# Optimization experiments

Measured on AMD Instinct MI355X. Metric: run time of the kernel, lower is better.

## Reference

```python
import jax, jax.numpy as jnp
import numpy as np

B, C, H, W = 8, 64, 128, 128


def setup_inputs() -> dict:
    key = jax.random.key(0)
    k1, k2, k3 = jax.random.split(key, 3)
    x = jax.random.normal(k1, (B, C, H, W), dtype=jnp.float32)
    # offset conv weights: (2C, C, 3, 3), small init like the module (std=0.01)
    W_off = jax.random.normal(k2, (2 * C, C, 3, 3), dtype=jnp.float32) * 0.01
    # following regular conv: (C_out, C, 3, 3)
    W_conv = jax.random.normal(k3, (C, C, 3, 3), dtype=jnp.float32) * 0.05
    b_conv = jnp.zeros((C,), dtype=jnp.float32)
    return {"x": x, "W_off": W_off, "W_conv": W_conv, "b_conv": b_conv}


def _conv2d_same(x, w):
    return jax.lax.conv_general_dilated(
        x, w, window_strides=(1, 1), padding=[(1, 1), (1, 1)],
        dimension_numbers=("NCHW", "OIHW", "NCHW"))


def _deform_offset(x, W_off):
    """Faithful ConvOffset2D: offset conv + clamped 4-corner bilinear gather."""
    b, c, h, w = x.shape
    offsets_ = _conv2d_same(x, W_off)                    # (b, 2c, h, w)
    # torch contiguous view (b,2c,h,w) -> (b*c, h*w, 2): adjacent w elements
    # become the 2 offset components; jnp.reshape matches this exactly.
    offsets = offsets_.reshape(b * c, h * w, 2)
    xf = x.reshape(b * c, h, w)

    gy, gx = jnp.meshgrid(jnp.arange(h), jnp.arange(w), indexing="ij")
    grid = jnp.stack([gy, gx], axis=-1).reshape(-1, 2).astype(x.dtype)  # (h*w, 2)
    coords = offsets + grid[None]                        # (b*c, h*w, 2)

    cy = jnp.clip(coords[..., 0], 0.0, h - 1)
    cx = jnp.clip(coords[..., 1], 0.0, w - 1)
    y0 = jnp.floor(cy)
    y1 = jnp.ceil(cy)
    x0 = jnp.floor(cx)
    x1 = jnp.ceil(cx)

    flat = xf.reshape(-1)                                # (b*c*h*w,)
    base = (jnp.arange(b * c, dtype=jnp.int32) * (h * w))[:, None]

    def gather(yy, xx):
        idx = base + yy.astype(jnp.int32) * w + xx.astype(jnp.int32)
        return flat[idx]

    v_lt = gather(y0, x0)   # (floor y, floor x)
    v_rb = gather(y1, x1)   # (ceil y,  ceil x)
    v_lb = gather(y0, x1)   # (floor y, ceil x)
    v_rt = gather(y1, x0)   # (ceil y,  floor x)

    dy = cy - y0
    dx = cx - x0
    v_t = dy * (v_rt - v_lt) + v_lt
    v_b = dy * (v_rb - v_lb) + v_lb
    out = dx * (v_b - v_t) + v_t                         # (b*c, h*w)
    return out.reshape(b, c, h, w)


def reference(x, W_off, W_conv, b_conv):
    x_def = _deform_offset(x, W_off)
    out = _conv2d_same(x_def, W_conv) + b_conv[None, :, None, None]
    return out
```

## Files before the change

### kernel.cpp

```cpp
#include <hip/hip_runtime.h>

#define DH 128
#define DW 128
#define DB 8
#define DC 64
constexpr int HW = DH * DW;

typedef __attribute__((ext_vector_type(4))) float f32x4;
typedef __attribute__((ext_vector_type(16))) float f32x16;
typedef __attribute__((ext_vector_type(8))) short bf16x8;
typedef __attribute__((ext_vector_type(4))) unsigned int u32x4;

__device__ __forceinline__ unsigned short f2b(float f) {
    unsigned int u = __builtin_bit_cast(unsigned int, f);
    u = (u + 0x7FFFu + ((u >> 16) & 1u)) >> 16;
    return (unsigned short)u;
}
__device__ __forceinline__ float b2f(unsigned short h) {
    unsigned int u = ((unsigned int)h) << 16;
    return __builtin_bit_cast(float, u);
}

__global__ __launch_bounds__(256) void xpose_kernel(
    const float* __restrict__ x, unsigned short* __restrict__ xh)
{
    __shared__ unsigned short sm[64 * 80];
    const int b = blockIdx.y;
    const int p0 = blockIdx.x * 64;
    const int t = threadIdx.x;
    const int ci = t >> 2, q = t & 3;
    const float* xr = x + ((size_t)b * 64 + ci) * HW + p0;
#pragma unroll
    for (int j = 0; j < 4; ++j) {
        int pix = (j * 4 + q) * 4;
        float4 v = *(const float4*)(xr + pix);
        sm[(pix + 0) * 80 + ci] = f2b(v.x);
        sm[(pix + 1) * 80 + ci] = f2b(v.y);
        sm[(pix + 2) * 80 + ci] = f2b(v.z);
        sm[(pix + 3) * 80 + ci] = f2b(v.w);
    }
    __syncthreads();
    unsigned short* outp = xh + ((size_t)b * HW + p0) * 64;
    for (int i = t; i < 512; i += 256) {
        int pix = i >> 3, cq = i & 7;
        u32x4 v = *(const u32x4*)(sm + pix * 80 + cq * 8);
        *(u32x4*)(outp + pix * 64 + cq * 8) = v;
    }
}

__global__ __launch_bounds__(256) void wprep_kernel(
    const float* __restrict__ wo, const float* __restrict__ wc,
    unsigned short* __restrict__ wt1, unsigned short* __restrict__ wt2)
{
    int id = blockIdx.x * 256 + threadIdx.x;
    const int N1 = 9 * 128 * 64, N2 = 9 * 64 * 64;
    if (id < N1) {
        int t = id / (128 * 64);
        int rem = id - t * 128 * 64;
        int co = rem >> 6, ci = rem & 63;
        wt1[id] = f2b(wo[(co * 64 + ci) * 9 + t]);
    } else if (id < N1 + N2) {
        int k = id - N1;
        int t = k / (64 * 64);
        int rem = k - t * 64 * 64;
        int co = rem >> 6, ci = rem & 63;
        wt2[k] = f2b(wc[(co * 64 + ci) * 9 + t]);
    }
}

template<int COUT, int MI, bool HWC_BF16_OUT>
__global__ __launch_bounds__(512, 4) void conv_mfma_kernel(
    const unsigned short* __restrict__ xh,
    const unsigned short* __restrict__ wt,
    const float* __restrict__ bias,
    void* __restrict__ outp)
{
    constexpr int WBYTES = COUT * 64 * 2;
    constexpr int SPASS = WBYTES / 8192;
    __shared__ char sm[41472 + 2 * WBYTES];
    char* const wbuf0 = sm + 41472;
    char* const wbuf1 = sm + 41472 + WBYTES;

    const int tid = threadIdx.x;
    const int b = blockIdx.y;
    const int ty0 = (blockIdx.x >> 3) << 4;
    const int tx0 = (blockIdx.x & 7) << 4;
    const unsigned short* xb = xh + (size_t)b * HW * 64;

    u32x4 wreg[SPASS];
    {
        const char* wsrc = (const char*)wt;
#pragma unroll
        for (int s = 0; s < SPASS; ++s) {
            int L = (s * 512 + tid) * 16;
            wreg[s] = *(const u32x4*)(wsrc + (L ^ (((L >> 7) & 7) << 4)));
        }
    }
    for (int i = tid; i < 2592; i += 512) {
        int hp = i >> 3, cq = i & 7;
        int hy = hp / 18, hx = hp - hy * 18;
        int gy = ty0 + hy - 1, gx = tx0 + hx - 1;
        u32x4 v = {0u, 0u, 0u, 0u};
        if ((unsigned)gy < 128u && (unsigned)gx < 128u)
            v = *(const u32x4*)(xb + (size_t)((gy << 7) + gx) * 64 + cq * 8);
        *(u32x4*)(sm + ((hp * 128 + cq * 16) ^ ((hp & 7) << 4))) = v;
    }
#pragma unroll
    for (int s = 0; s < SPASS; ++s) {
        int L = (s * 512 + tid) * 16;
        *(u32x4*)(wbuf0 + L) = wreg[s];
    }
    __syncthreads();

    const int lane = tid & 63;
    const int wv = tid >> 6;
    const int wm = wv & 1;
    const int wn = wv >> 1;
    const int n = lane & 31;
    const int half = lane >> 5;
    const int px = n & 15;
    const int pyb = wn * 4 + (n >> 4);
    const int swzA = (lane & 7) << 4;
    const int rowA = (wm * (MI * 32) + n) * 128 + half * 16;

    int hp0[2];
#pragma unroll
    for (int ni = 0; ni < 2; ++ni)
        hp0[ni] = (pyb + ni * 2) * 18 + px;

    f32x16 acc[MI][2];
#pragma unroll
    for (int mi = 0; mi < MI; ++mi)
#pragma unroll
        for (int ni = 0; ni < 2; ++ni)
#pragma unroll
            for (int e = 0; e < 16; ++e) acc[mi][ni][e] = 0.f;

#pragma unroll
    for (int t9 = 0; t9 < 9; ++t9) {
        const int toff = (t9 / 3) * 18 + (t9 % 3);
        const char* wb = (t9 & 1) ? wbuf1 : wbuf0;
        u32x4 wr[SPASS];
        if (t9 < 8) {
            const char* wsrc = (const char*)(wt + (size_t)(t9 + 1) * COUT * 64);
#pragma unroll
            for (int s = 0; s < SPASS; ++s) {
                int L = (s * 512 + tid) * 16;
                wr[s] = *(const u32x4*)(wsrc + (L ^ (((L >> 7) & 7) << 4)));
            }
        }
#pragma unroll
        for (int kk = 0; kk < 4; ++kk) {
            const int kcol = kk * 32;
            bf16x8 a[MI], bv[2];
#pragma unroll
            for (int mi = 0; mi < MI; ++mi)
                a[mi] = *(const bf16x8*)(wb + ((rowA + mi * 4096 + kcol) ^ swzA));
#pragma unroll
            for (int ni = 0; ni < 2; ++ni) {
                int hp = hp0[ni] + toff;
                bv[ni] = *(const bf16x8*)(sm + ((hp * 128 + kcol + half * 16) ^ ((hp & 7) << 4)));
            }
#pragma unroll
            for (int mi = 0; mi < MI; ++mi)
#pragma unroll
                for (int ni = 0; ni < 2; ++ni)
                    acc[mi][ni] = __builtin_amdgcn_mfma_f32_32x32x16_bf16(
                        a[mi], bv[ni], acc[mi][ni], 0, 0, 0);
        }
        if (t9 < 8) {
            char* wbn = ((t9 + 1) & 1) ? wbuf1 : wbuf0;
#pragma unroll
            for (int s = 0; s < SPASS; ++s) {
                int L = (s * 512 + tid) * 16;
                *(u32x4*)(wbn + L) = wr[s];
            }
        }
        __syncthreads();
    }

#pragma unroll
    for (int ni = 0; ni < 2; ++ni) {
        int py = pyb + ni * 2;
        int gp = (ty0 + py) * 128 + tx0 + px;
        if (HWC_BF16_OUT) {
            unsigned short* o = (unsigned short*)outp + ((size_t)b * HW + gp) * COUT;
#pragma unroll
            for (int mi = 0; mi < MI; ++mi) {
                int cob = wm * (MI * 32) + mi * 32 + half * 4;
#pragma unroll
                for (int g = 0; g < 4; ++g) {
                    uint2 pk;
                    pk.x = (unsigned)f2b(acc[mi][ni][g * 4 + 0]) |
                           ((unsigned)f2b(acc[mi][ni][g * 4 + 1]) << 16);
                    pk.y = (unsigned)f2b(acc[mi][ni][g * 4 + 2]) |
                           ((unsigned)f2b(acc[mi][ni][g * 4 + 3]) << 16);
                    *(uint2*)(o + cob + g * 8) = pk;
                }
            }
        } else {
            float* o = (float*)outp + (size_t)b * COUT * HW + gp;
#pragma unroll
            for (int mi = 0; mi < MI; ++mi) {
                int cob = wm * (MI * 32) + mi * 32 + half * 4;
#pragma unroll
                for (int g = 0; g < 4; ++g)
#pragma unroll
                    for (int r = 0; r < 4; ++r) {
                        int co = cob + g * 8 + r;
                        o[(size_t)co * HW] = acc[mi][ni][g * 4 + r] + bias[co];
                    }
            }
        }
    }
}

__global__ __launch_bounds__(256) void deform_kernel(
    const unsigned short* __restrict__ xh,
    const unsigned short* __restrict__ offs,
    unsigned short* __restrict__ xdef)
{
    int idx = blockIdx.x * 256 + threadIdx.x;
    int ci = idx & 63;
    int bp = idx >> 6;
    int p = bp & (HW - 1);
    int b = bp >> 14;
    int ch = 2 * ci + (p >> 13);
    int pp = (2 * p) & (HW - 1);
    const unsigned short* ob = offs + (size_t)b * HW * 128;
    float oy = b2f(ob[(size_t)pp * 128 + ch]);
    float ox = b2f(ob[(size_t)(pp + 1) * 128 + ch]);
    int gy = p >> 7, gx = p & 127;
    float cy = fminf(fmaxf(oy + (float)gy, 0.f), 127.f);
    float cx = fminf(fmaxf(ox + (float)gx, 0.f), 127.f);
    float y0f = floorf(cy), x0f = floorf(cx);
    int y0 = (int)y0f, x0i = (int)x0f;
    int y1 = (int)ceilf(cy), x1 = (int)ceilf(cx);
    const unsigned short* pl = xh + (size_t)b * HW * 64 + ci;
    float v_lt = b2f(pl[(size_t)(y0 * 128 + x0i) * 64]);
    float v_rb = b2f(pl[(size_t)(y1 * 128 + x1) * 64]);
    float v_lb = b2f(pl[(size_t)(y0 * 128 + x1) * 64]);
    float v_rt = b2f(pl[(size_t)(y1 * 128 + x0i) * 64]);
    float dy = cy - y0f, dx = cx - x0f;
    float v_t = fmaf(dy, v_rt - v_lt, v_lt);
    float v_b = fmaf(dy, v_rb - v_lb, v_lb);
    xdef[(size_t)bp * 64 + ci] = f2b(fmaf(dx, v_b - v_t, v_t));
}

extern "C" void kernel_launch(void* const* d_in, const int* in_sizes, int n_in,
                              void* d_out, int out_size, void* d_ws, size_t ws_size,
                              hipStream_t stream) {
    const float* x      = (const float*)d_in[0];
    const float* W_off  = (const float*)d_in[1];
    const float* W_conv = (const float*)d_in[2];
    const float* b_conv = (const float*)d_in[3];

    unsigned short* xh   = (unsigned short*)d_ws;
    unsigned short* offs = xh + (size_t)DB * HW * 64;
    unsigned short* xdef = offs + (size_t)DB * HW * 128;
    unsigned short* wt1  = xdef + (size_t)DB * HW * 64;
    unsigned short* wt2  = wt1 + 9 * 128 * 64;
    float* out = (float*)d_out;

    xpose_kernel<<<dim3(HW / 64, DB), 256, 0, stream>>>(x, xh);
    wprep_kernel<<<(9 * 128 * 64 + 9 * 64 * 64 + 255) / 256, 256, 0, stream>>>(
        W_off, W_conv, wt1, wt2);

    conv_mfma_kernel<128, 2, true><<<dim3(64, DB), 512, 0, stream>>>(
        xh, wt1, nullptr, offs);

    deform_kernel<<<(DB * HW * 64) / 256, 256, 0, stream>>>(xh, offs, xdef);

    conv_mfma_kernel<64, 1, false><<<dim3(64, DB), 512, 0, stream>>>(
        xdef, wt2, b_conv, out);
}
```

Measured before the change: 162.2 us.

## Fuse deformable bilinear sampling into second conv and merge prep kernels

The bilinear deformable gather now runs inside the second MFMA conv kernel, which writes the sampled halo tile straight into shared memory instead of going through a global xdef buffer. The transpose and weight-prep kernels are merged into one launch. This removes a global write and read of the deformed tensor plus two kernel launches. The cost is that halo pixels are recomputed per tile (18x18 for a 16x16 output), and the conv kernel's staging now does gather-heavy scattered loads.

```diff
diff --git a/kernel.cpp b/kernel.cpp
--- a/kernel.cpp
+++ b/kernel.cpp
@@ -21,50 +21,50 @@
     return __builtin_bit_cast(float, u);
 }
 
-__global__ __launch_bounds__(256) void xpose_kernel(
-    const float* __restrict__ x, unsigned short* __restrict__ xh)
-{
-    __shared__ unsigned short sm[64 * 80];
-    const int b = blockIdx.y;
-    const int p0 = blockIdx.x * 64;
-    const int t = threadIdx.x;
-    const int ci = t >> 2, q = t & 3;
-    const float* xr = x + ((size_t)b * 64 + ci) * HW + p0;
-#pragma unroll
-    for (int j = 0; j < 4; ++j) {
-        int pix = (j * 4 + q) * 4;
-        float4 v = *(const float4*)(xr + pix);
-        sm[(pix + 0) * 80 + ci] = f2b(v.x);
-        sm[(pix + 1) * 80 + ci] = f2b(v.y);
-        sm[(pix + 2) * 80 + ci] = f2b(v.z);
-        sm[(pix + 3) * 80 + ci] = f2b(v.w);
-    }
-    __syncthreads();
-    unsigned short* outp = xh + ((size_t)b * HW + p0) * 64;
-    for (int i = t; i < 512; i += 256) {
-        int pix = i >> 3, cq = i & 7;
-        u32x4 v = *(const u32x4*)(sm + pix * 80 + cq * 8);
-        *(u32x4*)(outp + pix * 64 + cq * 8) = v;
-    }
-}
-
-__global__ __launch_bounds__(256) void wprep_kernel(
-    const float* __restrict__ wo, const float* __restrict__ wc,
+__global__ __launch_bounds__(256) void prep_kernel(
+    const float* __restrict__ x, const float* __restrict__ wo,
+    const float* __restrict__ wc, unsigned short* __restrict__ xh,
     unsigned short* __restrict__ wt1, unsigned short* __restrict__ wt2)
 {
-    int id = blockIdx.x * 256 + threadIdx.x;
-    const int N1 = 9 * 128 * 64, N2 = 9 * 64 * 64;
-    if (id < N1) {
-        int t = id / (128 * 64);
-        int rem = id - t * 128 * 64;
-        int co = rem >> 6, ci = rem & 63;
-        wt1[id] = f2b(wo[(co * 64 + ci) * 9 + t]);
-    } else if (id < N1 + N2) {
-        int k = id - N1;
-        int t = k / (64 * 64);
-        int rem = k - t * 64 * 64;
-        int co = rem >> 6, ci = rem & 63;
-        wt2[k] = f2b(wc[(co * 64 + ci) * 9 + t]);
+    __shared__ unsigned short smx[64 * 80];
+    const int blk = blockIdx.x;
+    const int t = threadIdx.x;
+    if (blk < 2048) {
+        const int b = blk >> 8;
+        const int p0 = (blk & 255) * 64;
+        const int ci = t >> 2, q = t & 3;
+        const float* xr = x + ((size_t)b * 64 + ci) * HW + p0;
+#pragma unroll
+        for (int j = 0; j < 4; ++j) {
+            int pix = (j * 4 + q) * 4;
+            float4 v = *(const float4*)(xr + pix);
+            smx[(pix + 0) * 80 + ci] = f2b(v.x);
+            smx[(pix + 1) * 80 + ci] = f2b(v.y);
+            smx[(pix + 2) * 80 + ci] = f2b(v.z);
+            smx[(pix + 3) * 80 + ci] = f2b(v.w);
+        }
+        __syncthreads();
+        unsigned short* outp = xh + ((size_t)b * HW + p0) * 64;
+        for (int i = t; i < 512; i += 256) {
+            int pix = i >> 3, cq = i & 7;
+            u32x4 v = *(const u32x4*)(smx + pix * 80 + cq * 8);
+            *(u32x4*)(outp + pix * 64 + cq * 8) = v;
+        }
+    } else {
+        int id = (blk - 2048) * 256 + t;
+        const int N1 = 9 * 128 * 64, N2 = 9 * 64 * 64;
+        if (id < N1) {
+            int tp = id / (128 * 64);
+            int rem = id - tp * 128 * 64;
+            int co = rem >> 6, ci = rem & 63;
+            wt1[id] = f2b(wo[(co * 64 + ci) * 9 + tp]);
+        } else if (id < N1 + N2) {
+            int k = id - N1;
+            int tp = k / (64 * 64);
+            int rem = k - tp * 64 * 64;
+            int co = rem >> 6, ci = rem & 63;
+            wt2[k] = f2b(wc[(co * 64 + ci) * 9 + tp]);
+        }
     }
 }
 
@@ -215,36 +215,129 @@
     }
 }
 
-__global__ __launch_bounds__(256) void deform_kernel(
+__global__ __launch_bounds__(512, 4) void conv2_deform_kernel(
     const unsigned short* __restrict__ xh,
     const unsigned short* __restrict__ offs,
-    unsigned short* __restrict__ xdef)
+    const unsigned short* __restrict__ wt,
+    const float* __restrict__ bias,
+    float* __restrict__ out)
 {
-    int idx = blockIdx.x * 256 + threadIdx.x;
-    int ci = idx & 63;
-    int bp = idx >> 6;
-    int p = bp & (HW - 1);
-    int b = bp >> 14;
-    int ch = 2 * ci + (p >> 13);
-    int pp = (2 * p) & (HW - 1);
+    __shared__ char sm[41472 + 2 * 8192];
+    char* const wbuf0 = sm + 41472;
+    char* const wbuf1 = sm + 41472 + 8192;
+
+    const int tid = threadIdx.x;
+    const int b = blockIdx.y;
+    const int ty0 = (blockIdx.x >> 3) << 4;
+    const int tx0 = (blockIdx.x & 7) << 4;
+    const unsigned short* xb = xh + (size_t)b * HW * 64;
     const unsigned short* ob = offs + (size_t)b * HW * 128;
-    float oy = b2f(ob[(size_t)pp * 128 + ch]);
-    float ox = b2f(ob[(size_t)(pp + 1) * 128 + ch]);
-    int gy = p >> 7, gx = p & 127;
-    float cy = fminf(fmaxf(oy + (float)gy, 0.f), 127.f);
-    float cx = fminf(fmaxf(ox + (float)gx, 0.f), 127.f);
-    float y0f = floorf(cy), x0f = floorf(cx);
-    int y0 = (int)y0f, x0i = (int)x0f;
-    int y1 = (int)ceilf(cy), x1 = (int)ceilf(cx);
-    const unsigned short* pl = xh + (size_t)b * HW * 64 + ci;
-    float v_lt = b2f(pl[(size_t)(y0 * 128 + x0i) * 64]);
-    float v_rb = b2f(pl[(size_t)(y1 * 128 + x1) * 64]);
-    float v_lb = b2f(pl[(size_t)(y0 * 128 + x1) * 64]);
-    float v_rt = b2f(pl[(size_t)(y1 * 128 + x0i) * 64]);
-    float dy = cy - y0f, dx = cx - x0f;
-    float v_t = fmaf(dy, v_rt - v_lt, v_lt);
-    float v_b = fmaf(dy, v_rb - v_lb, v_lb);
-    xdef[(size_t)bp * 64 + ci] = f2b(fmaf(dx, v_b - v_t, v_t));
+
+    u32x4 wreg;
+    {
+        int L = tid * 16;
+        wreg = *(const u32x4*)((const char*)wt + (L ^ (((L >> 7) & 7) << 4)));
+    }
+
+    for (int i = tid; i < 324 * 64; i += 512) {
+        int hp = i >> 6, ci = i & 63;
+        int hy = hp / 18, hx = hp - hy * 18;
+        int gy = ty0 + hy - 1, gx = tx0 + hx - 1;
+        unsigned short val = 0;
+        if ((unsigned)gy < 128u && (unsigned)gx < 128u) {
+            int q = (gy << 7) + gx;
+            int ch = 2 * ci + (q >> 13);
+            int pp = (2 * q) & (HW - 1);
+            float oy = b2f(ob[(size_t)pp * 128 + ch]);
+            float ox = b2f(ob[(size_t)(pp + 1) * 128 + ch]);
+            float cy = fminf(fmaxf(oy + (float)gy, 0.f), 127.f);
+            float cx = fminf(fmaxf(ox + (float)gx, 0.f), 127.f);
+            float y0f = floorf(cy), x0f = floorf(cx);
+            int y0 = (int)y0f, x0i = (int)x0f;
+            int y1 = (int)ceilf(cy), x1 = (int)ceilf(cx);
+            const unsigned short* pl = xb + ci;
+            float v_lt = b2f(pl[(size_t)(y0 * 128 + x0i) * 64]);
+            float v_rb = b2f(pl[(size_t)(y1 * 128 + x1) * 64]);
+            float v_lb = b2f(pl[(size_t)(y0 * 128 + x1) * 64]);
+            float v_rt = b2f(pl[(size_t)(y1 * 128 + x0i) * 64]);
+            float dy = cy - y0f, dxf = cx - x0f;
+            float v_t = fmaf(dy, v_rt - v_lt, v_lt);
+            float v_b = fmaf(dy, v_rb - v_lb, v_lb);
+            val = f2b(fmaf(dxf, v_b - v_t, v_t));
+        }
+        *(unsigned short*)(sm + ((hp * 128 + ci * 2) ^ ((hp & 7) << 4))) = val;
+    }
+    *(u32x4*)(wbuf0 + tid * 16) = wreg;
+    __syncthreads();
+
+    const int lane = tid & 63;
+    const int wv = tid >> 6;
+    const int wm = wv & 1;
+    const int wn = wv >> 1;
+    const int n = lane & 31;
+    const int half = lane >> 5;
+    const int px = n & 15;
+    const int pyb = wn * 4 + (n >> 4);
+    const int swzA = (lane & 7) << 4;
+    const int rowA = (wm * 32 + n) * 128 + half * 16;
+
+    int hp0[2];
+#pragma unroll
+    for (int ni = 0; ni < 2; ++ni)
+        hp0[ni] = (pyb + ni * 2) * 18 + px;
+
+    f32x16 acc[2];
+#pragma unroll
+    for (int ni = 0; ni < 2; ++ni)
+#pragma unroll
+        for (int e = 0; e < 16; ++e) acc[ni][e] = 0.f;
+
+#pragma unroll
+    for (int t9 = 0; t9 < 9; ++t9) {
+        const int toff = (t9 / 3) * 18 + (t9 % 3);
+        const char* wb = (t9 & 1) ? wbuf1 : wbuf0;
+        u32x4 wr;
+        if (t9 < 8) {
+            const char* wsrc = (const char*)(wt + (size_t)(t9 + 1) * 64 * 64);
+            int L = tid * 16;
+            wr = *(const u32x4*)(wsrc + (L ^ (((L >> 7) & 7) << 4)));
+        }
+#pragma unroll
+        for (int kk = 0; kk < 4; ++kk) {
+            const int kcol = kk * 32;
+            bf16x8 a = *(const bf16x8*)(wb + ((rowA + kcol) ^ swzA));
+            bf16x8 bv[2];
+#pragma unroll
+            for (int ni = 0; ni < 2; ++ni) {
+                int hp = hp0[ni] + toff;
+                bv[ni] = *(const bf16x8*)(sm + ((hp * 128 + kcol + half * 16) ^ ((hp & 7) << 4)));
+            }
+#pragma unroll
+            for (int ni = 0; ni < 2; ++ni)
+                acc[ni] = __builtin_amdgcn_mfma_f32_32x32x16_bf16(
+                    a, bv[ni], acc[ni], 0, 0, 0);
+        }
+        if (t9 < 8) {
+            char* wbn = ((t9 + 1) & 1) ? wbuf1 : wbuf0;
+            *(u32x4*)(wbn + tid * 16) = wr;
+        }
+        __syncthreads();
+    }
+
+#pragma unroll
+    for (int ni = 0; ni < 2; ++ni) {
+        int py = pyb + ni * 2;
+        int gp = (ty0 + py) * 128 + tx0 + px;
+        float* o = out + (size_t)b * 64 * HW + gp;
+        int cob = wm * 32 + half * 4;
+#pragma unroll
+        for (int g = 0; g < 4; ++g)
+#pragma unroll
+            for (int r = 0; r < 4; ++r) {
+                int co = cob + g * 8 + r;
+                o[(size_t)co * HW] = acc[ni][g * 4 + r] + bias[co];
+            }
+    }
 }
 
 extern "C" void kernel_launch(void* const* d_in, const int* in_sizes, int n_in,
@@ -257,20 +350,15 @@
 
     unsigned short* xh   = (unsigned short*)d_ws;
     unsigned short* offs = xh + (size_t)DB * HW * 64;
-    unsigned short* xdef = offs + (size_t)DB * HW * 128;
-    unsigned short* wt1  = xdef + (size_t)DB * HW * 64;
+    unsigned short* wt1  = offs + (size_t)DB * HW * 128;
     unsigned short* wt2  = wt1 + 9 * 128 * 64;
     float* out = (float*)d_out;
 
-    xpose_kernel<<<dim3(HW / 64, DB), 256, 0, stream>>>(x, xh);
-    wprep_kernel<<<(9 * 128 * 64 + 9 * 64 * 64 + 255) / 256, 256, 0, stream>>>(
-        W_off, W_conv, wt1, wt2);
+    prep_kernel<<<2048 + 432, 256, 0, stream>>>(x, W_off, W_conv, xh, wt1, wt2);
 
     conv_mfma_kernel<128, 2, true><<<dim3(64, DB), 512, 0, stream>>>(
         xh, wt1, nullptr, offs);
 
-    deform_kernel<<<(DB * HW * 64) / 256, 256, 0, stream>>>(xh, offs, xdef);
-
-    conv_mfma_kernel<64, 1, false><<<dim3(64, DB), 512, 0, stream>>>(
-        xdef, wt2, b_conv, out);
-}
+    conv2_deform_kernel<<<dim3(64, DB), 512, 0, stream>>>(
+        xh, offs, wt2, b_conv, out);
+}
```

Result: no change. 163.3 us (+0.7%).
